# Kernel tuning notes

Measured on AMD Instinct MI355X. Metric: run time of the kernel, lower is better.

## Reference

```python
import jax, jax.numpy as jnp
import numpy as np

B, S, DM, H = 4, 4096, 1024, 16
HD = DM // H  # 64


def setup_inputs() -> dict:
    key = jax.random.key(0)
    ks = jax.random.split(key, 9)
    sc = 0.02
    x = jax.random.normal(ks[0], (B, S, DM), dtype=jnp.float32)
    Wq = jax.random.normal(ks[1], (DM, DM), dtype=jnp.float32) * sc
    bq = jnp.zeros((DM,), dtype=jnp.float32)
    Wk = jax.random.normal(ks[2], (DM, HD), dtype=jnp.float32) * sc
    bk = jnp.zeros((HD,), dtype=jnp.float32)
    Wv = jax.random.normal(ks[3], (DM, HD), dtype=jnp.float32) * sc
    bv = jnp.zeros((HD,), dtype=jnp.float32)
    Wo = jax.random.normal(ks[4], (DM, DM), dtype=jnp.float32) * sc
    bo = jnp.zeros((DM,), dtype=jnp.float32)
    return {"x": x, "Wq": Wq, "bq": bq, "Wk": Wk, "bk": bk,
            "Wv": Wv, "bv": bv, "Wo": Wo, "bo": bo}


def reference(x, Wq, bq, Wk, bk, Wv, bv, Wo, bo):
    b, s, _ = x.shape
    q = (x @ Wq + bq).reshape(b, s, H, HD)          # [B,S,H,D]
    k = (x @ Wk + bk)                                # [B,S,D] (single KV head)
    v = (x @ Wv + bv)                                # [B,S,D]
    # Faithful to source: k/v expanded over head axis, matmul over last two
    # dims of [B,S,H,D] -> scores are per-token head-vs-head: [B,S,H,H].
    k_e = jnp.broadcast_to(k[:, :, None, :], (b, s, H, HD))
    v_e = jnp.broadcast_to(v[:, :, None, :], (b, s, H, HD))
    scores = jnp.einsum('bshd,bsgd->bshg', q, k_e) / jnp.sqrt(jnp.float32(HD))
    attn = jax.nn.softmax(scores, axis=-1)           # uniform (scores const over g)
    out = jnp.einsum('bshg,bsgd->bshd', attn, v_e)   # [B,S,H,D]
    return out.reshape(b, s, DM) @ Wo + bo
```

## Files before the change

### kernel.cpp

```cpp
#include <hip/hip_runtime.h>

#define M_TOTAL 16384
#define DMODEL  1024
#define HDIM    64
#define NHEAD   16

typedef _Float16 half8 __attribute__((ext_vector_type(8)));
typedef float    f32x4 __attribute__((ext_vector_type(4)));

__global__ __launch_bounds__(256) void prep_kernel(const float* __restrict__ Wv,
                                                   const float* __restrict__ Wo,
                                                   _Float16* __restrict__ WvT,
                                                   _Float16* __restrict__ WosumT) {
    const int t = blockIdx.x * 256 + threadIdx.x;
    {
        const int d = t & 63, k = t >> 6;
        WvT[d * DMODEL + k] = (_Float16)Wv[k * HDIM + d];
    }
    {
        const int n = t & 1023, d = t >> 10;
        float s = 0.f;
        #pragma unroll
        for (int h = 0; h < NHEAD; ++h) s += Wo[(h * HDIM + d) * DMODEL + n];
        WosumT[n * HDIM + d] = (_Float16)s;
    }
}

#define XH_STRIDE 136
#define VH_STRIDE 72

__global__ __launch_bounds__(256) void mqa_fused(const float* __restrict__ X,
                                                 const float* __restrict__ bv,
                                                 const float* __restrict__ bo,
                                                 const _Float16* __restrict__ WvT,
                                                 const _Float16* __restrict__ WosumT,
                                                 float* __restrict__ Out) {
    __shared__ _Float16 Xh[16 * XH_STRIDE];
    __shared__ _Float16 Vh[16 * VH_STRIDE];

    const int tid = threadIdx.x;
    const int l   = tid & 63;
    const int w   = tid >> 6;
    const int lr  = l & 15;
    const int lk  = l >> 4;
    const int m0  = blockIdx.x * 16;

    f32x4 acc = {0.f, 0.f, 0.f, 0.f};
    for (int k0 = 0; k0 < DMODEL; k0 += 128) {
        #pragma unroll
        for (int i = 0; i < 2; ++i) {
            const int f4 = tid + i * 256;
            const int r  = f4 >> 5;
            const int c4 = f4 & 31;
            const float4 v = *(const float4*)&X[(size_t)(m0 + r) * DMODEL + k0 + c4 * 4];
            union { _Float16 h[4]; unsigned long long u; } p;
            p.h[0] = (_Float16)v.x; p.h[1] = (_Float16)v.y;
            p.h[2] = (_Float16)v.z; p.h[3] = (_Float16)v.w;
            *(unsigned long long*)&Xh[r * XH_STRIDE + c4 * 4] = p.u;
        }
        __syncthreads();
        #pragma unroll
        for (int ks = 0; ks < 4; ++ks) {
            const half8 a = *(const half8*)&Xh[lr * XH_STRIDE + ks * 32 + lk * 8];
            const half8 b = *(const half8*)&WvT[(size_t)(w * 16 + lr) * DMODEL + k0 + ks * 32 + lk * 8];
            acc = __builtin_amdgcn_mfma_f32_16x16x32_f16(a, b, acc, 0, 0, 0);
        }
        __syncthreads();
    }
    {
        const float bvv = bv[w * 16 + lr];
        #pragma unroll
        for (int j = 0; j < 4; ++j)
            Vh[(lk * 4 + j) * VH_STRIDE + w * 16 + lr] = (_Float16)(acc[j] + bvv);
    }
    __syncthreads();

    const half8 a0 = *(const half8*)&Vh[lr * VH_STRIDE + lk * 8];
    const half8 a1 = *(const half8*)&Vh[lr * VH_STRIDE + 32 + lk * 8];
    #pragma unroll 4
    for (int nf = 0; nf < 16; ++nf) {
        const int n0 = w * 256 + nf * 16;
        const half8 b0 = *(const half8*)&WosumT[(size_t)(n0 + lr) * HDIM + lk * 8];
        const half8 b1 = *(const half8*)&WosumT[(size_t)(n0 + lr) * HDIM + 32 + lk * 8];
        f32x4 o = {0.f, 0.f, 0.f, 0.f};
        o = __builtin_amdgcn_mfma_f32_16x16x32_f16(a0, b0, o, 0, 0, 0);
        o = __builtin_amdgcn_mfma_f32_16x16x32_f16(a1, b1, o, 0, 0, 0);
        const float bov = bo[n0 + lr];
        #pragma unroll
        for (int j = 0; j < 4; ++j)
            Out[(size_t)(m0 + lk * 4 + j) * DMODEL + n0 + lr] = o[j] + bov;
    }
}

extern "C" void kernel_launch(void* const* d_in, const int* in_sizes, int n_in,
                              void* d_out, int out_size, void* d_ws, size_t ws_size,
                              hipStream_t stream) {
    const float* x  = (const float*)d_in[0];
    const float* Wv = (const float*)d_in[5];
    const float* bv = (const float*)d_in[6];
    const float* Wo = (const float*)d_in[7];
    const float* bo = (const float*)d_in[8];

    _Float16* WvT    = (_Float16*)d_ws;
    _Float16* WosumT = (_Float16*)((char*)d_ws + 64 * 1024 * 2);
    float*    out    = (float*)d_out;

    prep_kernel<<<256, 256, 0, stream>>>(Wv, Wo, WvT, WosumT);
    mqa_fused<<<M_TOTAL / 16, 256, 0, stream>>>(x, bv, bo, WvT, WosumT, out);
}
```

Measured before the change: 49.86 us.

## Stage the full 16-row X tile in LDS with all loads issued upfront

Replaces the k-chunked loop, which loaded 128 columns of X, synced, ran the MFMAs and synced again, with a single prologue. Each thread now issues all of its 16 float4 global loads at once, converts them to fp16 and writes them into an LDS tile that holds all 1024 columns. One barrier follows, then the full K-loop of MFMAs runs. This exposes more memory-level parallelism and removes 15 barriers, at the cost of about 33KB of LDS and 64 extra registers per thread, which may reduce occupancy.

```diff
diff --git a/kernel.cpp b/kernel.cpp
--- a/kernel.cpp
+++ b/kernel.cpp
@@ -26,7 +26,7 @@
     }
 }
 
-#define XH_STRIDE 136
+#define XH_STRIDE 1032
 #define VH_STRIDE 72
 
 __global__ __launch_bounds__(256) void mqa_fused(const float* __restrict__ X,
@@ -45,27 +45,40 @@
     const int lk  = l >> 4;
     const int m0  = blockIdx.x * 16;
 
+    float4 xa[8], xb[8];
+    #pragma unroll
+    for (int j = 0; j < 8; ++j) {
+        const int slot = j * 256 + tid;
+        const int r    = slot >> 7;
+        const int c    = (slot & 127) * 8;
+        const float* p = &X[(size_t)(m0 + r) * DMODEL + c];
+        xa[j] = *(const float4*)p;
+        xb[j] = *(const float4*)(p + 4);
+    }
+    #pragma unroll
+    for (int j = 0; j < 8; ++j) {
+        const int slot = j * 256 + tid;
+        const int r    = slot >> 7;
+        const int c    = (slot & 127) * 8;
+        union { _Float16 h[8]; half8 v; } pk;
+        pk.h[0] = (_Float16)xa[j].x; pk.h[1] = (_Float16)xa[j].y;
+        pk.h[2] = (_Float16)xa[j].z; pk.h[3] = (_Float16)xa[j].w;
+        pk.h[4] = (_Float16)xb[j].x; pk.h[5] = (_Float16)xb[j].y;
+        pk.h[6] = (_Float16)xb[j].z; pk.h[7] = (_Float16)xb[j].w;
+        *(half8*)&Xh[r * XH_STRIDE + c] = pk.v;
+    }
+    __syncthreads();
+
     f32x4 acc = {0.f, 0.f, 0.f, 0.f};
-    for (int k0 = 0; k0 < DMODEL; k0 += 128) {
-        #pragma unroll
-        for (int i = 0; i < 2; ++i) {
-            const int f4 = tid + i * 256;
-            const int r  = f4 >> 5;
-            const int c4 = f4 & 31;
-            const float4 v = *(const float4*)&X[(size_t)(m0 + r) * DMODEL + k0 + c4 * 4];
-            union { _Float16 h[4]; unsigned long long u; } p;
-            p.h[0] = (_Float16)v.x; p.h[1] = (_Float16)v.y;
-            p.h[2] = (_Float16)v.z; p.h[3] = (_Float16)v.w;
-            *(unsigned long long*)&Xh[r * XH_STRIDE + c4 * 4] = p.u;
-        }
-        __syncthreads();
-        #pragma unroll
-        for (int ks = 0; ks < 4; ++ks) {
-            const half8 a = *(const half8*)&Xh[lr * XH_STRIDE + ks * 32 + lk * 8];
-            const half8 b = *(const half8*)&WvT[(size_t)(w * 16 + lr) * DMODEL + k0 + ks * 32 + lk * 8];
+    {
+        const _Float16* xp  = &Xh[lr * XH_STRIDE + lk * 8];
+        const _Float16* wvp = &WvT[(size_t)(w * 16 + lr) * DMODEL + lk * 8];
+        #pragma unroll 8
+        for (int ks = 0; ks < 32; ++ks) {
+            const half8 a = *(const half8*)(xp + ks * 32);
+            const half8 b = *(const half8*)(wvp + ks * 32);
             acc = __builtin_amdgcn_mfma_f32_16x16x32_f16(a, b, acc, 0, 0, 0);
         }
-        __syncthreads();
     }
     {
         const float bvv = bv[w * 16 + lr];
```

Result: slower. 51.92 us (+4.1%).

## Split fused kernel into V-projection and output-projection kernels with register-pipelined loads

Applied to the files above, without the earlier changes.

Replaces the single fused kernel with two kernels. The first computes V = X·Wv with each wave owning 16 rows and all 64 output columns. It loads X straight into registers with a four-slot software prefetch, so the LDS staging and barriers go away. The second reads the fp16 V from workspace and does the Wosum output projection. This is meant to remove the per-chunk __syncthreads and LDS round trips and to reuse each A fragment across four MFMAs, at the cost of an extra kernel launch and a V write and read through global memory.

```diff
diff --git a/kernel.cpp b/kernel.cpp
--- a/kernel.cpp
+++ b/kernel.cpp
@@ -26,18 +26,59 @@
     }
 }
 
-#define XH_STRIDE 136
-#define VH_STRIDE 72
+__global__ __launch_bounds__(256) void vproj_kernel(const float* __restrict__ X,
+                                                    const float* __restrict__ bv,
+                                                    const _Float16* __restrict__ WvT,
+                                                    _Float16* __restrict__ V) {
+    const int tid = threadIdx.x;
+    const int l   = tid & 63;
+    const int w   = tid >> 6;
+    const int lr  = l & 15;
+    const int lk  = l >> 4;
+    const int m0  = (blockIdx.x * 4 + w) * 16;
 
-__global__ __launch_bounds__(256) void mqa_fused(const float* __restrict__ X,
-                                                 const float* __restrict__ bv,
-                                                 const float* __restrict__ bo,
-                                                 const _Float16* __restrict__ WvT,
-                                                 const _Float16* __restrict__ WosumT,
-                                                 float* __restrict__ Out) {
-    __shared__ _Float16 Xh[16 * XH_STRIDE];
-    __shared__ _Float16 Vh[16 * VH_STRIDE];
+    const float* xrow = X + (size_t)(m0 + lr) * DMODEL + lk * 8;
 
+    f32x4 acc[4] = {};
+    float4 abuf[4][2];
+    #pragma unroll
+    for (int s = 0; s < 4; ++s) {
+        abuf[s][0] = *(const float4*)(xrow + s * 32);
+        abuf[s][1] = *(const float4*)(xrow + s * 32 + 4);
+    }
+    #pragma unroll 4
+    for (int s = 0; s < 32; ++s) {
+        const int slot = s & 3;
+        const float4 x0 = abuf[slot][0];
+        const float4 x1 = abuf[slot][1];
+        if (s < 28) {
+            abuf[slot][0] = *(const float4*)(xrow + (s + 4) * 32);
+            abuf[slot][1] = *(const float4*)(xrow + (s + 4) * 32 + 4);
+        }
+        union { _Float16 h[8]; half8 v; } pk;
+        pk.h[0] = (_Float16)x0.x; pk.h[1] = (_Float16)x0.y;
+        pk.h[2] = (_Float16)x0.z; pk.h[3] = (_Float16)x0.w;
+        pk.h[4] = (_Float16)x1.x; pk.h[5] = (_Float16)x1.y;
+        pk.h[6] = (_Float16)x1.z; pk.h[7] = (_Float16)x1.w;
+        #pragma unroll
+        for (int n4 = 0; n4 < 4; ++n4) {
+            const half8 b = *(const half8*)&WvT[(size_t)(n4 * 16 + lr) * DMODEL + s * 32 + lk * 8];
+            acc[n4] = __builtin_amdgcn_mfma_f32_16x16x32_f16(pk.v, b, acc[n4], 0, 0, 0);
+        }
+    }
+    #pragma unroll
+    for (int n4 = 0; n4 < 4; ++n4) {
+        const float bvv = bv[n4 * 16 + lr];
+        #pragma unroll
+        for (int j = 0; j < 4; ++j)
+            V[(size_t)(m0 + lk * 4 + j) * HDIM + n4 * 16 + lr] = (_Float16)(acc[n4][j] + bvv);
+    }
+}
+
+__global__ __launch_bounds__(256) void oproj_kernel(const _Float16* __restrict__ V,
+                                                    const float* __restrict__ bo,
+                                                    const _Float16* __restrict__ WosumT,
+                                                    float* __restrict__ Out) {
     const int tid = threadIdx.x;
     const int l   = tid & 63;
     const int w   = tid >> 6;
@@ -45,44 +86,16 @@
     const int lk  = l >> 4;
     const int m0  = blockIdx.x * 16;
 
-    f32x4 acc = {0.f, 0.f, 0.f, 0.f};
-    for (int k0 = 0; k0 < DMODEL; k0 += 128) {
-        #pragma unroll
-        for (int i = 0; i < 2; ++i) {
-            const int f4 = tid + i * 256;
-            const int r  = f4 >> 5;
-            const int c4 = f4 & 31;
-            const float4 v = *(const float4*)&X[(size_t)(m0 + r) * DMODEL + k0 + c4 * 4];
-            union { _Float16 h[4]; unsigned long long u; } p;
-            p.h[0] = (_Float16)v.x; p.h[1] = (_Float16)v.y;
-            p.h[2] = (_Float16)v.z; p.h[3] = (_Float16)v.w;
-            *(unsigned long long*)&Xh[r * XH_STRIDE + c4 * 4] = p.u;
-        }
-        __syncthreads();
-        #pragma unroll
-        for (int ks = 0; ks < 4; ++ks) {
-            const half8 a = *(const half8*)&Xh[lr * XH_STRIDE + ks * 32 + lk * 8];
-            const half8 b = *(const half8*)&WvT[(size_t)(w * 16 + lr) * DMODEL + k0 + ks * 32 + lk * 8];
-            acc = __builtin_amdgcn_mfma_f32_16x16x32_f16(a, b, acc, 0, 0, 0);
-        }
-        __syncthreads();
-    }
-    {
-        const float bvv = bv[w * 16 + lr];
-        #pragma unroll
-        for (int j = 0; j < 4; ++j)
-            Vh[(lk * 4 + j) * VH_STRIDE + w * 16 + lr] = (_Float16)(acc[j] + bvv);
-    }
-    __syncthreads();
+    const _Float16* vp = V + (size_t)(m0 + lr) * HDIM + lk * 8;
+    const half8 a0 = *(const half8*)vp;
+    const half8 a1 = *(const half8*)(vp + 32);
 
-    const half8 a0 = *(const half8*)&Vh[lr * VH_STRIDE + lk * 8];
-    const half8 a1 = *(const half8*)&Vh[lr * VH_STRIDE + 32 + lk * 8];
     #pragma unroll 4
     for (int nf = 0; nf < 16; ++nf) {
         const int n0 = w * 256 + nf * 16;
         const half8 b0 = *(const half8*)&WosumT[(size_t)(n0 + lr) * HDIM + lk * 8];
         const half8 b1 = *(const half8*)&WosumT[(size_t)(n0 + lr) * HDIM + 32 + lk * 8];
-        f32x4 o = {0.f, 0.f, 0.f, 0.f};
+        f32x4 o = {};
         o = __builtin_amdgcn_mfma_f32_16x16x32_f16(a0, b0, o, 0, 0, 0);
         o = __builtin_amdgcn_mfma_f32_16x16x32_f16(a1, b1, o, 0, 0, 0);
         const float bov = bo[n0 + lr];
@@ -103,8 +116,10 @@
 
     _Float16* WvT    = (_Float16*)d_ws;
     _Float16* WosumT = (_Float16*)((char*)d_ws + 64 * 1024 * 2);
+    _Float16* V      = (_Float16*)((char*)d_ws + 256 * 1024);
     float*    out    = (float*)d_out;
 
     prep_kernel<<<256, 256, 0, stream>>>(Wv, Wo, WvT, WosumT);
-    mqa_fused<<<M_TOTAL / 16, 256, 0, stream>>>(x, bv, bo, WvT, WosumT, out);
+    vproj_kernel<<<M_TOTAL / 64, 256, 0, stream>>>(x, bv, WvT, V);
+    oproj_kernel<<<M_TOTAL / 16, 256, 0, stream>>>(V, bo, WosumT, out);
 }
```

After: 62.03 us. +24.4%, slower.

## Split-K V projection across waves with register-staged X and LDS-coalesced output stores

Applied to the files above, without the earlier changes.

The X·Wv projection now gives each wave a 256-wide K slice, loading X straight into registers and converting to fp16 there, instead of staging it through LDS with syncs on every K step. The four partial V tiles are reduced through an LDS buffer. The output projection writes through LDS so each lane can store contiguous float4 values to global memory, replacing strided scalar stores. A launch-bounds occupancy hint is added, in exchange for more registers (16 float4 of X per thread) and extra LDS round trips.

```diff
diff --git a/kernel.cpp b/kernel.cpp
--- a/kernel.cpp
+++ b/kernel.cpp
@@ -26,17 +26,15 @@
     }
 }
 
-#define XH_STRIDE 136
-#define VH_STRIDE 72
+#define VP_S 68
 
-__global__ __launch_bounds__(256) void mqa_fused(const float* __restrict__ X,
-                                                 const float* __restrict__ bv,
-                                                 const float* __restrict__ bo,
-                                                 const _Float16* __restrict__ WvT,
-                                                 const _Float16* __restrict__ WosumT,
-                                                 float* __restrict__ Out) {
-    __shared__ _Float16 Xh[16 * XH_STRIDE];
-    __shared__ _Float16 Vh[16 * VH_STRIDE];
+__global__ __launch_bounds__(256, 4) void mqa_fused(const float* __restrict__ X,
+                                                    const float* __restrict__ bv,
+                                                    const float* __restrict__ bo,
+                                                    const _Float16* __restrict__ WvT,
+                                                    const _Float16* __restrict__ WosumT,
+                                                    float* __restrict__ Out) {
+    __shared__ float Vp[4][16][VP_S];
 
     const int tid = threadIdx.x;
     const int l   = tid & 63;
@@ -44,51 +42,82 @@
     const int lr  = l & 15;
     const int lk  = l >> 4;
     const int m0  = blockIdx.x * 16;
+    const int k0  = w * 256;
 
-    f32x4 acc = {0.f, 0.f, 0.f, 0.f};
-    for (int k0 = 0; k0 < DMODEL; k0 += 128) {
+    const float* xp = X + (size_t)(m0 + lr) * DMODEL + k0 + lk * 8;
+    f32x4 xb[16];
+    #pragma unroll
+    for (int s = 0; s < 8; ++s) {
+        xb[2 * s]     = *(const f32x4*)(xp + s * 32);
+        xb[2 * s + 1] = *(const f32x4*)(xp + s * 32 + 4);
+    }
+    f32x4 acc[4] = {};
+    #pragma unroll
+    for (int s = 0; s < 8; ++s) {
+        union { _Float16 h[8]; half8 v; } pk;
+        const f32x4 x0 = xb[2 * s], x1 = xb[2 * s + 1];
         #pragma unroll
-        for (int i = 0; i < 2; ++i) {
-            const int f4 = tid + i * 256;
-            const int r  = f4 >> 5;
-            const int c4 = f4 & 31;
-            const float4 v = *(const float4*)&X[(size_t)(m0 + r) * DMODEL + k0 + c4 * 4];
-            union { _Float16 h[4]; unsigned long long u; } p;
-            p.h[0] = (_Float16)v.x; p.h[1] = (_Float16)v.y;
-            p.h[2] = (_Float16)v.z; p.h[3] = (_Float16)v.w;
-            *(unsigned long long*)&Xh[r * XH_STRIDE + c4 * 4] = p.u;
+        for (int j = 0; j < 4; ++j) {
+            pk.h[j]     = (_Float16)x0[j];
+            pk.h[4 + j] = (_Float16)x1[j];
         }
-        __syncthreads();
         #pragma unroll
-        for (int ks = 0; ks < 4; ++ks) {
-            const half8 a = *(const half8*)&Xh[lr * XH_STRIDE + ks * 32 + lk * 8];
-            const half8 b = *(const half8*)&WvT[(size_t)(w * 16 + lr) * DMODEL + k0 + ks * 32 + lk * 8];
-            acc = __builtin_amdgcn_mfma_f32_16x16x32_f16(a, b, acc, 0, 0, 0);
+        for (int n4 = 0; n4 < 4; ++n4) {
+            const half8 b = *(const half8*)&WvT[(size_t)(n4 * 16 + lr) * DMODEL + k0 + s * 32 + lk * 8];
+            acc[n4] = __builtin_amdgcn_mfma_f32_16x16x32_f16(pk.v, b, acc[n4], 0, 0, 0);
         }
-        __syncthreads();
     }
-    {
-        const float bvv = bv[w * 16 + lr];
+    #pragma unroll
+    for (int n4 = 0; n4 < 4; ++n4)
         #pragma unroll
         for (int j = 0; j < 4; ++j)
-            Vh[(lk * 4 + j) * VH_STRIDE + w * 16 + lr] = (_Float16)(acc[j] + bvv);
+            Vp[w][lk * 4 + j][n4 * 16 + lr] = acc[n4][j];
+    __syncthreads();
+
+    f32x4 s0a = {}, s0b = {}, s1a = {}, s1b = {};
+    #pragma unroll
+    for (int p = 0; p < 4; ++p) {
+        s0a += *(const f32x4*)&Vp[p][lr][lk * 8];
+        s0b += *(const f32x4*)&Vp[p][lr][lk * 8 + 4];
+        s1a += *(const f32x4*)&Vp[p][lr][32 + lk * 8];
+        s1b += *(const f32x4*)&Vp[p][lr][32 + lk * 8 + 4];
+    }
+    s0a += *(const f32x4*)&bv[lk * 8];
+    s0b += *(const f32x4*)&bv[lk * 8 + 4];
+    s1a += *(const f32x4*)&bv[32 + lk * 8];
+    s1b += *(const f32x4*)&bv[32 + lk * 8 + 4];
+    union { _Float16 h[8]; half8 v; } A0, A1;
+    #pragma unroll
+    for (int j = 0; j < 4; ++j) {
+        A0.h[j] = (_Float16)s0a[j]; A0.h[4 + j] = (_Float16)s0b[j];
+        A1.h[j] = (_Float16)s1a[j]; A1.h[4 + j] = (_Float16)s1b[j];
     }
     __syncthreads();
 
-    const half8 a0 = *(const half8*)&Vh[lr * VH_STRIDE + lk * 8];
-    const half8 a1 = *(const half8*)&Vh[lr * VH_STRIDE + 32 + lk * 8];
-    #pragma unroll 4
-    for (int nf = 0; nf < 16; ++nf) {
-        const int n0 = w * 256 + nf * 16;
-        const half8 b0 = *(const half8*)&WosumT[(size_t)(n0 + lr) * HDIM + lk * 8];
-        const half8 b1 = *(const half8*)&WosumT[(size_t)(n0 + lr) * HDIM + 32 + lk * 8];
-        f32x4 o = {0.f, 0.f, 0.f, 0.f};
-        o = __builtin_amdgcn_mfma_f32_16x16x32_f16(a0, b0, o, 0, 0, 0);
-        o = __builtin_amdgcn_mfma_f32_16x16x32_f16(a1, b1, o, 0, 0, 0);
-        const float bov = bo[n0 + lr];
+    float* ost = &Vp[w][0][0];
+    const int rr = l >> 2;
+    const int cc = (l & 3) * 4;
+    #pragma unroll
+    for (int g = 0; g < 4; ++g) {
+        const int nbase = w * 256 + g * 64;
         #pragma unroll
-        for (int j = 0; j < 4; ++j)
-            Out[(size_t)(m0 + lk * 4 + j) * DMODEL + n0 + lr] = o[j] + bov;
+        for (int t = 0; t < 4; ++t) {
+            const int n0 = nbase + t * 16;
+            const half8 b0 = *(const half8*)&WosumT[(size_t)(n0 + lr) * HDIM + lk * 8];
+            const half8 b1 = *(const half8*)&WosumT[(size_t)(n0 + lr) * HDIM + 32 + lk * 8];
+            f32x4 o = {};
+            o = __builtin_amdgcn_mfma_f32_16x16x32_f16(A0.v, b0, o, 0, 0, 0);
+            o = __builtin_amdgcn_mfma_f32_16x16x32_f16(A1.v, b1, o, 0, 0, 0);
+            #pragma unroll
+            for (int j = 0; j < 4; ++j)
+                ost[(lk * 4 + j) * VP_S + t * 16 + lr] = o[j];
+        }
+        #pragma unroll
+        for (int j = 0; j < 4; ++j) {
+            const f32x4 ov  = *(const f32x4*)&ost[rr * VP_S + cc + j * 16];
+            const f32x4 bo4 = *(const f32x4*)&bo[nbase + cc + j * 16];
+            *(f32x4*)&Out[(size_t)(m0 + rr) * DMODEL + nbase + cc + j * 16] = ov + bo4;
+        }
     }
 }
 
```

Measured after the change: 53.32 us. 1.07x slower.
